# Optimization experiments

Measured on AMD Instinct MI355X. Metric: run time of the kernel, lower is better.

The kernel has to match this reference:

```python
import jax, jax.numpy as jnp
import numpy as np

N = 50000
D = 256
E = 800000


def setup_inputs() -> dict:
    key = jax.random.key(0)
    ks = jax.random.split(key, 8)
    x = jax.random.normal(ks[0], (N, D), dtype=jnp.float32)
    edge_index = jax.random.randint(ks[1], (2, E), 0, N, dtype=jnp.int64)
    s = 1.0 / np.sqrt(D)
    # SAGEConv layer 0 params: lin_l (neighbors, with bias), lin_r (root, no bias)
    Wl0 = jax.random.uniform(ks[2], (D, D), jnp.float32, -s, s)
    bl0 = jnp.zeros((D,), jnp.float32)
    Wr0 = jax.random.uniform(ks[3], (D, D), jnp.float32, -s, s)
    # SAGEConv layer 1 params
    Wl1 = jax.random.uniform(ks[4], (D, D), jnp.float32, -s, s)
    bl1 = jnp.zeros((D,), jnp.float32)
    Wr1 = jax.random.uniform(ks[5], (D, D), jnp.float32, -s, s)
    return {"x": x, "edge_index": edge_index, "Wl0": Wl0, "bl0": bl0, "Wr0": Wr0,
            "Wl1": Wl1, "bl1": bl1, "Wr1": Wr1}


def _sage_conv(x, edge_index, Wl, bl, Wr):
    # PyG SAGEConv, aggr='mean': out = lin_l(mean_{j in N(i)} x_j) + lin_r(x_i)
    src, dst = edge_index[0], edge_index[1]
    msg = x[src]                                            # [E, D] gather
    agg = jax.ops.segment_sum(msg, dst, num_segments=x.shape[0])
    cnt = jax.ops.segment_sum(jnp.ones((edge_index.shape[1],), x.dtype), dst,
                              num_segments=x.shape[0])
    mean = agg / jnp.maximum(cnt, 1.0)[:, None]             # zero-degree -> 0
    return mean @ Wl + bl + x @ Wr


def reference(x, edge_index, Wl0, bl0, Wr0, Wl1, bl1, Wr1):
    negative_slope = 0.5
    target = x  # full-graph path: target nodes = all nodes
    h = x
    # dropout p=0.0 -> identity
    h = _sage_conv(h, edge_index, Wl0, bl0, Wr0)
    h = jnp.where(h >= 0, h, negative_slope * h)
    h = _sage_conv(h, edge_index, Wl1, bl1, Wr1)
    h = jnp.where(h >= 0, h, negative_slope * h)
    return (h, target)
```

## Files before the change

kernel.cpp:

```cpp
#include <hip/hip_runtime.h>
#include <hip/hip_fp8.h>


typedef __attribute__((ext_vector_type(8))) short bf16x8;
typedef __attribute__((ext_vector_type(4))) float f32x4;

__device__ __forceinline__ float bf2f(unsigned short b) {
    union { unsigned u; float f; } x; x.u = ((unsigned)b) << 16; return x.f;
}
__device__ __forceinline__ short f2bf(float f) {
    union { float f; unsigned u; } x; x.f = f;
    unsigned r = x.u + 0x7fffu + ((x.u >> 16) & 1u);
    return (short)(r >> 16);
}
__device__ __forceinline__ unsigned char f2fp8(float f) {
    __hip_fp8_e4m3 q(f);
    return (unsigned char)q.__x;
}
__device__ __forceinline__ float fp82f(unsigned char b) {
    __hip_fp8_e4m3 q; q.__x = (__hip_fp8_storage_t)b;
    return (float)q;
}


__global__ __launch_bounds__(512) void bkhist_prep_kernel(
    const int* __restrict__ ei, int* __restrict__ histT,
    int E, int NBK, int NCH, int CH,
    const float* __restrict__ x, short* __restrict__ xb,
    unsigned char* __restrict__ xq, float* __restrict__ xcopy,
    const float* __restrict__ Wl0, const float* __restrict__ Wr0,
    const float* __restrict__ Wl1, const float* __restrict__ Wr1,
    short* __restrict__ B1T, short* __restrict__ B2T, int total8) {
    if ((int)blockIdx.x < NCH) {
        __shared__ int h[512];
        int c = blockIdx.x;
        int base_e = c * CH;
        int nloc = E - base_e;
        if (nloc > CH) nloc = CH;
        h[threadIdx.x] = 0;
        __syncthreads();
        for (int t = threadIdx.x; t < nloc; t += 512)
            atomicAdd(&h[ei[E + base_e + t] >> 7], 1);
        __syncthreads();
        if ((int)threadIdx.x < NBK) histT[threadIdx.x * 128 + c] = h[threadIdx.x];
    } else {
        int gid = ((int)blockIdx.x - NCH) * 512 + threadIdx.x;
        if (gid < total8) {
            const float* p = x + (size_t)gid * 8;
            float4 v0 = *reinterpret_cast<const float4*>(p);
            float4 v1 = *reinterpret_cast<const float4*>(p + 4);
            bf16x8 t;
            t[0] = f2bf(v0.x); t[1] = f2bf(v0.y); t[2] = f2bf(v0.z); t[3] = f2bf(v0.w);
            t[4] = f2bf(v1.x); t[5] = f2bf(v1.y); t[6] = f2bf(v1.z); t[7] = f2bf(v1.w);
            *reinterpret_cast<bf16x8*>(xb + (size_t)gid * 8) = t;
            uchar4 q0, q1;
            q0.x = f2fp8(v0.x); q0.y = f2fp8(v0.y); q0.z = f2fp8(v0.z); q0.w = f2fp8(v0.w);
            q1.x = f2fp8(v1.x); q1.y = f2fp8(v1.y); q1.z = f2fp8(v1.z); q1.w = f2fp8(v1.w);
            *reinterpret_cast<uchar4*>(xq + (size_t)gid * 8) = q0;
            *reinterpret_cast<uchar4*>(xq + (size_t)gid * 8 + 4) = q1;
            *reinterpret_cast<float4*>(xcopy + (size_t)gid * 8) = v0;
            *reinterpret_cast<float4*>(xcopy + (size_t)gid * 8 + 4) = v1;
        } else {
            int idx = gid - total8;
            if (idx < 262144) {
                int sel = idx >> 17;
                int j = idx & 131071;
                int n = j >> 9;
                int k = j & 511;
                const float* Wl = sel ? Wl1 : Wl0;
                const float* Wr = sel ? Wr1 : Wr0;
                float v = (k < 256) ? Wl[k * 256 + n] : Wr[(k - 256) * 256 + n];
                (sel ? B2T : B1T)[j] = f2bf(v);
            }
        }
    }
}

__global__ __launch_bounds__(256) void scanA_kernel(
    int* __restrict__ histT, int* __restrict__ bktot, int NBK, int NCH) {
    int waveid = blockIdx.x * 4 + (threadIdx.x >> 6);
    int lane = threadIdx.x & 63;
    if (waveid >= NBK) return;
    int b = waveid;
    int v0 = (lane < NCH) ? histT[b * 128 + lane] : 0;
    int v1 = (64 + lane < NCH) ? histT[b * 128 + 64 + lane] : 0;
    int s0 = v0;
    #pragma unroll
    for (int d = 1; d < 64; d <<= 1) {
        int t = __shfl_up(s0, d, 64);
        if (lane >= d) s0 += t;
    }
    int t0 = __shfl(s0, 63, 64);
    int s1 = v1;
    #pragma unroll
    for (int d = 1; d < 64; d <<= 1) {
        int t = __shfl_up(s1, d, 64);
        if (lane >= d) s1 += t;
    }
    s1 += t0;
    if (lane < NCH) histT[b * 128 + lane] = s0 - v0;
    if (64 + lane < NCH) histT[b * 128 + 64 + lane] = s1 - v1;
    if (lane == 63) bktot[b] = __shfl(s1, 63, 64);
}

__global__ __launch_bounds__(512) void scanB_kernel(
    const int* __restrict__ bktot, int* __restrict__ bkoff,
    int* __restrict__ offs, int NBK, int N, int E) {
    __shared__ int sm[512];
    int tid = threadIdx.x;
    int v = (tid < NBK) ? bktot[tid] : 0;
    sm[tid] = v;
    __syncthreads();
    for (int off = 1; off < 512; off <<= 1) {
        int t = (tid >= off) ? sm[tid - off] : 0;
        __syncthreads();
        sm[tid] += t;
        __syncthreads();
    }
    if (tid < NBK) bkoff[tid] = sm[tid] - v;
    if (tid == 0) {
        bkoff[NBK] = E;
        offs[N] = E;
    }
}

__global__ __launch_bounds__(512) void binA_kernel(
    const int* __restrict__ ei, const int* __restrict__ histT,
    const int* __restrict__ bkoff, long long* __restrict__ pairs,
    int E, int NBK, int CH) {
    __shared__ int pos[512];
    int c = blockIdx.x;
    if ((int)threadIdx.x < NBK)
        pos[threadIdx.x] = histT[threadIdx.x * 128 + c] + bkoff[threadIdx.x];
    __syncthreads();
    int base_e = c * CH;
    int nloc = E - base_e;
    if (nloc > CH) nloc = CH;
    for (int t = threadIdx.x; t < nloc; t += 512) {
        int dst = ei[E + base_e + t];
        int src = ei[base_e + t];
        int p = atomicAdd(&pos[dst >> 7], 1);
        pairs[p] = ((long long)dst << 32) | (unsigned)src;
    }
}

__global__ __launch_bounds__(256) void binB_kernel(
    const long long* __restrict__ pairs, const int* __restrict__ bkoff,
    int* __restrict__ offs, float* __restrict__ invdeg,
    int* __restrict__ csr, int NBK, int N) {
    __shared__ int cnt[128];
    __shared__ int cur[128];
    int b = blockIdx.x;
    int t = threadIdx.x;
    if (t < 128) cnt[t] = 0;
    __syncthreads();
    int beg = bkoff[b];
    int end = bkoff[b + 1];
    for (int i = beg + t; i < end; i += 256)
        atomicAdd(&cnt[((int)(pairs[i] >> 32)) & 127], 1);
    __syncthreads();
    if (t < 64) {
        int c0 = cnt[2 * t], c1 = cnt[2 * t + 1];
        int s = c0 + c1;
        int incl = s;
        #pragma unroll
        for (int d = 1; d < 64; d <<= 1) {
            int x = __shfl_up(incl, d, 64);
            if (t >= d) incl += x;
        }
        int excl = incl - s;
        cur[2 * t] = beg + excl;
        cur[2 * t + 1] = beg + excl + c0;
    }
    __syncthreads();
    if (t < 128) {
        int node = (b << 7) + t;
        if (node < N) {
            offs[node] = cur[t];
            invdeg[node] = 1.0f / (float)(cnt[t] > 0 ? cnt[t] : 1);
        }
    }
    __syncthreads();
    for (int i = beg + t; i < end; i += 256) {
        long long p = pairs[i];
        int pos = atomicAdd(&cur[((int)(p >> 32)) & 127], 1);
        csr[pos] = (int)(p & 0xffffffffLL);
    }
}

__global__ __launch_bounds__(256) void agg_kernel(
    const unsigned char* __restrict__ feat,
    const int* __restrict__ offs, const int* __restrict__ csr,
    const float* __restrict__ invdeg,
    short* __restrict__ outp, int N) {
    int wave = threadIdx.x >> 6;
    int lane = threadIdx.x & 63;
    int node = blockIdx.x * 4 + wave;
    if (node >= N) return;
    int beg = offs[node];
    int end = offs[node + 1];
    int c = lane * 4;

    float a[4][4];
    #pragma unroll
    for (int u = 0; u < 4; ++u)
        #pragma unroll
        for (int k = 0; k < 4; ++k) a[u][k] = 0.f;

    int deg = end - beg;
    int n8 = deg & ~7;
    for (int t = 0; t < n8; t += 8) {
        int s0 = csr[beg + t];     int s1 = csr[beg + t + 1];
        int s2 = csr[beg + t + 2]; int s3 = csr[beg + t + 3];
        int s4 = csr[beg + t + 4]; int s5 = csr[beg + t + 5];
        int s6 = csr[beg + t + 6]; int s7 = csr[beg + t + 7];
        unsigned u0 = *reinterpret_cast<const unsigned*>(feat + (size_t)s0 * 256 + c);
        unsigned u1 = *reinterpret_cast<const unsigned*>(feat + (size_t)s1 * 256 + c);
        unsigned u2 = *reinterpret_cast<const unsigned*>(feat + (size_t)s2 * 256 + c);
        unsigned u3 = *reinterpret_cast<const unsigned*>(feat + (size_t)s3 * 256 + c);
        unsigned u4 = *reinterpret_cast<const unsigned*>(feat + (size_t)s4 * 256 + c);
        unsigned u5 = *reinterpret_cast<const unsigned*>(feat + (size_t)s5 * 256 + c);
        unsigned u6 = *reinterpret_cast<const unsigned*>(feat + (size_t)s6 * 256 + c);
        unsigned u7 = *reinterpret_cast<const unsigned*>(feat + (size_t)s7 * 256 + c);
        #pragma unroll
        for (int k = 0; k < 4; ++k) a[0][k] += fp82f((u0 >> (8 * k)) & 0xff);
        #pragma unroll
        for (int k = 0; k < 4; ++k) a[1][k] += fp82f((u1 >> (8 * k)) & 0xff);
        #pragma unroll
        for (int k = 0; k < 4; ++k) a[2][k] += fp82f((u2 >> (8 * k)) & 0xff);
        #pragma unroll
        for (int k = 0; k < 4; ++k) a[3][k] += fp82f((u3 >> (8 * k)) & 0xff);
        #pragma unroll
        for (int k = 0; k < 4; ++k) a[0][k] += fp82f((u4 >> (8 * k)) & 0xff);
        #pragma unroll
        for (int k = 0; k < 4; ++k) a[1][k] += fp82f((u5 >> (8 * k)) & 0xff);
        #pragma unroll
        for (int k = 0; k < 4; ++k) a[2][k] += fp82f((u6 >> (8 * k)) & 0xff);
        #pragma unroll
        for (int k = 0; k < 4; ++k) a[3][k] += fp82f((u7 >> (8 * k)) & 0xff);
    }
    for (int e = beg + n8; e < end; ++e) {
        int s = csr[e];
        unsigned u = *reinterpret_cast<const unsigned*>(feat + (size_t)s * 256 + c);
        #pragma unroll
        for (int k = 0; k < 4; ++k) a[0][k] += fp82f((u >> (8 * k)) & 0xff);
    }
    float inv = invdeg[node];
    short4 o;
    o.x = f2bf((a[0][0] + a[1][0] + a[2][0] + a[3][0]) * inv);
    o.y = f2bf((a[0][1] + a[1][1] + a[2][1] + a[3][1]) * inv);
    o.z = f2bf((a[0][2] + a[1][2] + a[2][2] + a[3][2]) * inv);
    o.w = f2bf((a[0][3] + a[1][3] + a[2][3] + a[3][3]) * inv);
    *reinterpret_cast<short4*>(&outp[(size_t)node * 256 + c]) = o;
}

template <int OUT_MODE>
__global__ __launch_bounds__(1024, 4) void gemm_kernel(
    const short* __restrict__ AL, const short* __restrict__ AR,
    const short* __restrict__ BT, const float* __restrict__ bias,
    void* __restrict__ Cout, unsigned char* __restrict__ Cq,
    int M, int ntiles) {
    __shared__ short ldsA[2][32 * 512];
    int wave = threadIdx.x >> 6;
    int lane = threadIdx.x & 63;
    int l16 = lane & 15;
    int lhi = lane >> 4;
    int c0 = wave * 16;

    bf16x8 breg[16];
    #pragma unroll
    for (int kk = 0; kk < 16; ++kk)
        breg[kk] = *reinterpret_cast<const bf16x8*>(
            &BT[(size_t)(c0 + l16) * 512 + kk * 32 + lhi * 8]);
    float bc = bias[c0 + l16];

    auto STAGE = [&](int tt, int buf) {
        #pragma unroll
        for (int i = 0; i < 2; ++i) {
            int r = i * 16 + wave;
            int grow = tt * 32 + r;
            if (grow >= M) grow = M - 1;
            int csw = (lane * 8) ^ ((r & 15) << 3);
            const short* src = (csw < 256)
                ? AL + (size_t)grow * 256 + csw
                : AR + (size_t)grow * 256 + (csw - 256);
            __builtin_amdgcn_global_load_lds(
                (const __attribute__((address_space(1))) unsigned int*)src,
                (__attribute__((address_space(3))) unsigned int*)
                    &ldsA[buf][r * 512],
                16, 0, 0);
        }
    };

    int t = blockIdx.x;
    int stride = gridDim.x;
    if (t >= ntiles) return;
    STAGE(t, 0);
    int buf = 0;
    int it = 0;
    for (; t < ntiles; t += stride, ++it) {
        int tn = t + stride;
        bool havenext = (tn < ntiles);
        if (havenext) STAGE(tn, buf ^ 1);

        if (it == 0) {
            if (havenext) asm volatile("s_waitcnt vmcnt(2)" ::: "memory");
            else          asm volatile("s_waitcnt vmcnt(0)" ::: "memory");
        } else if (havenext) {
            if constexpr (OUT_MODE == 0)
                asm volatile("s_waitcnt vmcnt(18)" ::: "memory");
            else
                asm volatile("s_waitcnt vmcnt(10)" ::: "memory");
        } else {
            if constexpr (OUT_MODE == 0)
                asm volatile("s_waitcnt vmcnt(16)" ::: "memory");
            else
                asm volatile("s_waitcnt vmcnt(8)" ::: "memory");
        }
        __builtin_amdgcn_s_barrier();
        __builtin_amdgcn_sched_barrier(0);

        int row0 = t * 32;
        f32x4 acc[2];
        acc[0] = (f32x4){0.f, 0.f, 0.f, 0.f};
        acc[1] = (f32x4){0.f, 0.f, 0.f, 0.f};

        const short* lb = &ldsA[buf][0];
        #pragma unroll
        for (int kk = 0; kk < 16; ++kk) {
            bf16x8 a0, a1;
            {
                int r = l16;
                int ks = (kk * 32 + lhi * 8) ^ ((r & 15) << 3);
                a0 = *reinterpret_cast<const bf16x8*>(&lb[r * 512 + ks]);
            }
            {
                int r = 16 + l16;
                int ks = (kk * 32 + lhi * 8) ^ ((r & 15) << 3);
                a1 = *reinterpret_cast<const bf16x8*>(&lb[r * 512 + ks]);
            }
            acc[0] = __builtin_amdgcn_mfma_f32_16x16x32_bf16(
                a0, breg[kk], acc[0], 0, 0, 0);
            acc[1] = __builtin_amdgcn_mfma_f32_16x16x32_bf16(
                a1, breg[kk], acc[1], 0, 0, 0);
        }

        #pragma unroll
        for (int mt = 0; mt < 2; ++mt) {
            #pragma unroll
            for (int r = 0; r < 4; ++r) {
                int grow = row0 + mt * 16 + lhi * 4 + r;
                if (grow >= M) grow = M - 1;
                int gcol = c0 + l16;
                float v = acc[mt][r] + bc;
                v = (v >= 0.f) ? v : 0.5f * v;
                if (OUT_MODE == 0) {
                    ((short*)Cout)[(size_t)grow * 256 + gcol] = f2bf(v);
                    Cq[(size_t)grow * 256 + gcol] = f2fp8(v);
                } else {
                    ((float*)Cout)[(size_t)grow * 256 + gcol] = v;
                }
            }
        }
        __builtin_amdgcn_s_barrier();
        buf ^= 1;
    }
}


extern "C" void kernel_launch(void* const* d_in, const int* in_sizes, int n_in,
                              void* d_out, int out_size, void* d_ws, size_t ws_size,
                              hipStream_t stream) {
    const float* x   = (const float*)d_in[0];
    const int*   ei  = (const int*)d_in[1];
    const float* Wl0 = (const float*)d_in[2];
    const float* bl0 = (const float*)d_in[3];
    const float* Wr0 = (const float*)d_in[4];
    const float* Wl1 = (const float*)d_in[5];
    const float* bl1 = (const float*)d_in[6];
    const float* Wr1 = (const float*)d_in[7];

    const int N = in_sizes[0] / 256;
    const int E = in_sizes[1] / 2;
    const int NBK = (N + 127) / 128;
    int CH = 8192;
    while ((E + CH - 1) / CH > 128) CH <<= 1;
    const int NCH = (E + CH - 1) / CH;

    char* ws = (char*)d_ws;
    size_t o = 0;
    auto alloc = [&](size_t bytes) {
        size_t p = o;
        o = (o + bytes + 255) & ~(size_t)255;
        return p;
    };
    int*   offs   = (int*)  (ws + alloc((size_t)(N + 1) * 4));
    float* invdeg = (float*)(ws + alloc((size_t)N * 4));
    int*   histT  = (int*)  (ws + alloc((size_t)512 * 128 * 4));
    int*   bktot  = (int*)  (ws + alloc(512 * 4));
    int*   bkoff  = (int*)  (ws + alloc(((size_t)NBK + 1) * 4));
    long long* pairs = (long long*)(ws + alloc((size_t)E * 8));
    int*   csr    = (int*)  (ws + alloc((size_t)E * 4));
    short* xb     = (short*)(ws + alloc((size_t)N * 256 * 2));
    short* meanb  = (short*)(ws + alloc((size_t)N * 256 * 2));
    short* h0     = (short*)(ws + alloc((size_t)N * 256 * 2));
    unsigned char* xq  = (unsigned char*)(ws + alloc((size_t)N * 256));
    unsigned char* h0q = (unsigned char*)(ws + alloc((size_t)N * 256));
    short* B1T    = (short*)(ws + alloc(262144));
    short* B2T    = (short*)(ws + alloc(262144));

    int total8 = N * 32;
    int prep_blocks = (total8 + 262144 + 511) / 512;
    bkhist_prep_kernel<<<NCH + prep_blocks, 512, 0, stream>>>(
        ei, histT, E, NBK, NCH, CH,
        x, xb, xq, (float*)d_out + (size_t)N * 256,
        Wl0, Wr0, Wl1, Wr1, B1T, B2T, total8);
    scanA_kernel<<<(NBK + 3) / 4, 256, 0, stream>>>(histT, bktot, NBK, NCH);
    scanB_kernel<<<1, 512, 0, stream>>>(bktot, bkoff, offs, NBK, N, E);
    binA_kernel<<<NCH, 512, 0, stream>>>(ei, histT, bkoff, pairs, E, NBK, CH);
    binB_kernel<<<NBK, 256, 0, stream>>>(pairs, bkoff, offs, invdeg, csr, NBK, N);

    int ab = (N + 3) / 4;
    int ntiles = (N + 31) / 32;
    int gblocks = 512;
    agg_kernel<<<ab, 256, 0, stream>>>(xq, offs, csr, invdeg, meanb, N);
    gemm_kernel<0><<<gblocks, 1024, 0, stream>>>(
        meanb, xb, B1T, bl0, h0, h0q, N, ntiles);
    agg_kernel<<<ab, 256, 0, stream>>>(h0q, offs, csr, invdeg, meanb, N);
    gemm_kernel<1><<<gblocks, 1024, 0, stream>>>(
        meanb, h0, B2T, bl1, d_out, nullptr, N, ntiles);
}
```

Before: 219.4 us.

## Drop bf16 h0 copy, read fp8 root features in layer-1 GEMM, pack CSR pairs

Layer 0's GEMM no longer writes a bf16 copy of h0. Layer 1's GEMM now reads the fp8 h0q for its root term, dequantises it in registers and writes it into a split LDS buffer. The binning pairs are packed into 32 bits (local dst in the high bits, src in the low 25 bits), which halves that scratch traffic. The GEMM pipeline switches from fine-grained vmcnt waits to full drains at the end of each iteration. The cost is extra fp8 precision loss in the root path, and a src limit of 2^25 nodes.

```diff
diff --git a/kernel.cpp b/kernel.cpp
--- a/kernel.cpp
+++ b/kernel.cpp
@@ -126,7 +126,7 @@
 
 __global__ __launch_bounds__(512) void binA_kernel(
     const int* __restrict__ ei, const int* __restrict__ histT,
-    const int* __restrict__ bkoff, long long* __restrict__ pairs,
+    const int* __restrict__ bkoff, unsigned* __restrict__ pairs,
     int E, int NBK, int CH) {
     __shared__ int pos[512];
     int c = blockIdx.x;
@@ -140,12 +140,12 @@
         int dst = ei[E + base_e + t];
         int src = ei[base_e + t];
         int p = atomicAdd(&pos[dst >> 7], 1);
-        pairs[p] = ((long long)dst << 32) | (unsigned)src;
+        pairs[p] = ((unsigned)(dst & 127) << 25) | (unsigned)src;
     }
 }
 
 __global__ __launch_bounds__(256) void binB_kernel(
-    const long long* __restrict__ pairs, const int* __restrict__ bkoff,
+    const unsigned* __restrict__ pairs, const int* __restrict__ bkoff,
     int* __restrict__ offs, float* __restrict__ invdeg,
     int* __restrict__ csr, int NBK, int N) {
     __shared__ int cnt[128];
@@ -157,7 +157,7 @@
     int beg = bkoff[b];
     int end = bkoff[b + 1];
     for (int i = beg + t; i < end; i += 256)
-        atomicAdd(&cnt[((int)(pairs[i] >> 32)) & 127], 1);
+        atomicAdd(&cnt[pairs[i] >> 25], 1);
     __syncthreads();
     if (t < 64) {
         int c0 = cnt[2 * t], c1 = cnt[2 * t + 1];
@@ -182,9 +182,9 @@
     }
     __syncthreads();
     for (int i = beg + t; i < end; i += 256) {
-        long long p = pairs[i];
-        int pos = atomicAdd(&cur[((int)(p >> 32)) & 127], 1);
-        csr[pos] = (int)(p & 0xffffffffLL);
+        unsigned p = pairs[i];
+        int pos = atomicAdd(&cur[p >> 25], 1);
+        csr[pos] = (int)(p & 0x1FFFFFFu);
     }
 }
 
@@ -256,16 +256,19 @@
 
 template <int OUT_MODE>
 __global__ __launch_bounds__(1024, 4) void gemm_kernel(
-    const short* __restrict__ AL, const short* __restrict__ AR,
+    const short* __restrict__ AL, const void* __restrict__ ARv,
     const short* __restrict__ BT, const float* __restrict__ bias,
-    void* __restrict__ Cout, unsigned char* __restrict__ Cq,
+    float* __restrict__ Cout, unsigned char* __restrict__ Cq,
     int M, int ntiles) {
-    __shared__ short ldsA[2][32 * 512];
+    __shared__ short ldsAL[2][32 * 256];
+    __shared__ short ldsAR[2][32 * 256];
     int wave = threadIdx.x >> 6;
     int lane = threadIdx.x & 63;
     int l16 = lane & 15;
     int lhi = lane >> 4;
     int c0 = wave * 16;
+    int rsub = lane >> 5;
+    int jcol = (lane & 31) * 8;
 
     bf16x8 breg[16];
     #pragma unroll
@@ -274,76 +277,84 @@
             &BT[(size_t)(c0 + l16) * 512 + kk * 32 + lhi * 8]);
     float bc = bias[c0 + l16];
 
+    const short* ARb = (const short*)ARv;
+    const unsigned char* ARq = (const unsigned char*)ARv;
+    uint2 nq;
+
     auto STAGE = [&](int tt, int buf) {
-        #pragma unroll
-        for (int i = 0; i < 2; ++i) {
-            int r = i * 16 + wave;
-            int grow = tt * 32 + r;
-            if (grow >= M) grow = M - 1;
-            int csw = (lane * 8) ^ ((r & 15) << 3);
-            const short* src = (csw < 256)
-                ? AL + (size_t)grow * 256 + csw
-                : AR + (size_t)grow * 256 + (csw - 256);
+        int r = 2 * wave + rsub;
+        int grow = tt * 32 + r;
+        if (grow >= M) grow = M - 1;
+        int swz = (r & 15) << 3;
+        const short* srcA = AL + (size_t)grow * 256 + (jcol ^ swz);
+        __builtin_amdgcn_global_load_lds(
+            (const __attribute__((address_space(1))) unsigned int*)srcA,
+            (__attribute__((address_space(3))) unsigned int*)
+                &ldsAL[buf][2 * wave * 256], 16, 0, 0);
+        if (OUT_MODE == 0) {
+            const short* srcB = ARb + (size_t)grow * 256 + (jcol ^ swz);
             __builtin_amdgcn_global_load_lds(
-                (const __attribute__((address_space(1))) unsigned int*)src,
+                (const __attribute__((address_space(1))) unsigned int*)srcB,
                 (__attribute__((address_space(3))) unsigned int*)
-                    &ldsA[buf][r * 512],
-                16, 0, 0);
-        }
+                    &ldsAR[buf][2 * wave * 256], 16, 0, 0);
+        } else {
+            nq = *reinterpret_cast<const uint2*>(
+                ARq + (size_t)grow * 256 + (jcol ^ swz));
+        }
+    };
+    auto WRITE_AR = [&](int buf) {
+        int r = 2 * wave + rsub;
+        bf16x8 w;
+        #pragma unroll
+        for (int k = 0; k < 4; ++k)
+            w[k] = f2bf(fp82f((nq.x >> (8 * k)) & 0xff));
+        #pragma unroll
+        for (int k = 0; k < 4; ++k)
+            w[4 + k] = f2bf(fp82f((nq.y >> (8 * k)) & 0xff));
+        *reinterpret_cast<bf16x8*>(&ldsAR[buf][r * 256 + jcol]) = w;
     };
 
     int t = blockIdx.x;
     int stride = gridDim.x;
     if (t >= ntiles) return;
+
     STAGE(t, 0);
+    asm volatile("s_waitcnt vmcnt(0)" ::: "memory");
+    if (OUT_MODE == 1) {
+        WRITE_AR(0);
+        asm volatile("s_waitcnt lgkmcnt(0)" ::: "memory");
+    }
+    __builtin_amdgcn_s_barrier();
+    __builtin_amdgcn_sched_barrier(0);
+
     int buf = 0;
-    int it = 0;
-    for (; t < ntiles; t += stride, ++it) {
+    for (; t < ntiles; t += stride) {
         int tn = t + stride;
         bool havenext = (tn < ntiles);
         if (havenext) STAGE(tn, buf ^ 1);
-
-        if (it == 0) {
-            if (havenext) asm volatile("s_waitcnt vmcnt(2)" ::: "memory");
-            else          asm volatile("s_waitcnt vmcnt(0)" ::: "memory");
-        } else if (havenext) {
-            if constexpr (OUT_MODE == 0)
-                asm volatile("s_waitcnt vmcnt(18)" ::: "memory");
-            else
-                asm volatile("s_waitcnt vmcnt(10)" ::: "memory");
-        } else {
-            if constexpr (OUT_MODE == 0)
-                asm volatile("s_waitcnt vmcnt(16)" ::: "memory");
-            else
-                asm volatile("s_waitcnt vmcnt(8)" ::: "memory");
-        }
-        __builtin_amdgcn_s_barrier();
-        __builtin_amdgcn_sched_barrier(0);
 
         int row0 = t * 32;
         f32x4 acc[2];
         acc[0] = (f32x4){0.f, 0.f, 0.f, 0.f};
         acc[1] = (f32x4){0.f, 0.f, 0.f, 0.f};
 
-        const short* lb = &ldsA[buf][0];
         #pragma unroll
         for (int kk = 0; kk < 16; ++kk) {
-            bf16x8 a0, a1;
-            {
-                int r = l16;
-                int ks = (kk * 32 + lhi * 8) ^ ((r & 15) << 3);
-                a0 = *reinterpret_cast<const bf16x8*>(&lb[r * 512 + ks]);
-            }
-            {
-                int r = 16 + l16;
-                int ks = (kk * 32 + lhi * 8) ^ ((r & 15) << 3);
-                a1 = *reinterpret_cast<const bf16x8*>(&lb[r * 512 + ks]);
-            }
+            const short* lb = (kk < 8) ? &ldsAL[buf][0] : &ldsAR[buf][0];
+            int kb = (kk & 7) * 32 + lhi * 8;
+            int swz0 = (l16 & 15) << 3;
+            bf16x8 a0 = *reinterpret_cast<const bf16x8*>(
+                &lb[l16 * 256 + (kb ^ swz0)]);
+            bf16x8 a1 = *reinterpret_cast<const bf16x8*>(
+                &lb[(16 + l16) * 256 + (kb ^ swz0)]);
             acc[0] = __builtin_amdgcn_mfma_f32_16x16x32_bf16(
                 a0, breg[kk], acc[0], 0, 0, 0);
             acc[1] = __builtin_amdgcn_mfma_f32_16x16x32_bf16(
                 a1, breg[kk], acc[1], 0, 0, 0);
         }
+
+        asm volatile("s_waitcnt vmcnt(0)" ::: "memory");
+        if (OUT_MODE == 1 && havenext) WRITE_AR(buf ^ 1);
 
         #pragma unroll
         for (int mt = 0; mt < 2; ++mt) {
@@ -355,14 +366,16 @@
                 float v = acc[mt][r] + bc;
                 v = (v >= 0.f) ? v : 0.5f * v;
                 if (OUT_MODE == 0) {
-                    ((short*)Cout)[(size_t)grow * 256 + gcol] = f2bf(v);
                     Cq[(size_t)grow * 256 + gcol] = f2fp8(v);
                 } else {
-                    ((float*)Cout)[(size_t)grow * 256 + gcol] = v;
+                    Cout[(size_t)grow * 256 + gcol] = v;
                 }
             }
         }
+        if (OUT_MODE == 1)
+            asm volatile("s_waitcnt lgkmcnt(0)" ::: "memory");
         __builtin_amdgcn_s_barrier();
+        __builtin_amdgcn_sched_barrier(0);
         buf ^= 1;
     }
 }
@@ -399,11 +412,10 @@
     int*   histT  = (int*)  (ws + alloc((size_t)512 * 128 * 4));
     int*   bktot  = (int*)  (ws + alloc(512 * 4));
     int*   bkoff  = (int*)  (ws + alloc(((size_t)NBK + 1) * 4));
-    long long* pairs = (long long*)(ws + alloc((size_t)E * 8));
+    unsigned* pairs = (unsigned*)(ws + alloc((size_t)E * 4));
     int*   csr    = (int*)  (ws + alloc((size_t)E * 4));
     short* xb     = (short*)(ws + alloc((size_t)N * 256 * 2));
     short* meanb  = (short*)(ws + alloc((size_t)N * 256 * 2));
-    short* h0     = (short*)(ws + alloc((size_t)N * 256 * 2));
     unsigned char* xq  = (unsigned char*)(ws + alloc((size_t)N * 256));
     unsigned char* h0q = (unsigned char*)(ws + alloc((size_t)N * 256));
     short* B1T    = (short*)(ws + alloc(262144));
@@ -425,8 +437,8 @@
     int gblocks = 512;
     agg_kernel<<<ab, 256, 0, stream>>>(xq, offs, csr, invdeg, meanb, N);
     gemm_kernel<0><<<gblocks, 1024, 0, stream>>>(
-        meanb, xb, B1T, bl0, h0, h0q, N, ntiles);
+        meanb, xb, B1T, bl0, nullptr, h0q, N, ntiles);
     agg_kernel<<<ab, 256, 0, stream>>>(h0q, offs, csr, invdeg, meanb, N);
     gemm_kernel<1><<<gblocks, 1024, 0, stream>>>(
-        meanb, h0, B2T, bl1, d_out, nullptr, N, ntiles);
-}
+        meanb, h0q, B2T, bl1, (float*)d_out, nullptr, N, ntiles);
+}
```

Measured after the change: 218.2 us. Within noise of the previous version (-0.5%).
